# Performance work log

Hardware: AMD Instinct MI355X
Metric: run time of the kernel (lower is better)

Reference implementation:

```python
import jax, jax.numpy as jnp
import numpy as np

EMBED_DIM = 1024
NUM_HEADS = 16
HEAD_DIM = EMBED_DIM // NUM_HEADS
BATCH = 2
SEQ = 2048


def setup_inputs() -> dict:
    key = jax.random.key(0)
    ks = jax.random.split(key, 9)
    scale = 1.0 / np.sqrt(EMBED_DIM)
    return {
        "inputs": jax.random.normal(ks[0], (BATCH, SEQ, EMBED_DIM), jnp.float32),
        "Wq": jax.random.normal(ks[1], (EMBED_DIM, EMBED_DIM), jnp.float32) * scale,
        "bq": jnp.zeros((EMBED_DIM,), jnp.float32),
        "Wk": jax.random.normal(ks[2], (EMBED_DIM, EMBED_DIM), jnp.float32) * scale,
        "bk": jnp.zeros((EMBED_DIM,), jnp.float32),
        "Wv": jax.random.normal(ks[3], (EMBED_DIM, EMBED_DIM), jnp.float32) * scale,
        "bv": jnp.zeros((EMBED_DIM,), jnp.float32),
        "Wo": jax.random.normal(ks[4], (EMBED_DIM, EMBED_DIM), jnp.float32) * scale,
        "bo": jnp.zeros((EMBED_DIM,), jnp.float32),
    }


def reference(inputs, Wq, bq, Wk, bk, Wv, bv, Wo, bo):
    B, S, D = inputs.shape
    H, Dh = NUM_HEADS, HEAD_DIM

    def split_heads(x):  # [B,S,D] -> [B,H,S,Dh]
        return x.reshape(B, S, H, Dh).transpose(0, 2, 1, 3)

    Q = split_heads(inputs @ Wq + bq)
    K = split_heads(inputs @ Wk + bk)
    V = split_heads(inputs @ Wv + bv)

    # naive full-score attention, faithful to the original
    scores = jnp.einsum("bhqd,bhkd->bhqk", Q, K) / jnp.sqrt(jnp.float32(Dh))
    weights = jax.nn.softmax(scores, axis=-1)
    out = jnp.einsum("bhqk,bhkd->bhqd", weights, V)

    concat = out.transpose(0, 2, 1, 3).reshape(B, S, D)
    return concat @ Wo + bo
```

## Files before the change

### kernel.cpp

```cpp
#include <hip/hip_runtime.h>

#define EMBED 1024
#define NHEAD 16
#define HDIM  64
#define BATCH 2
#define SEQ   2048
#define MTOK  (BATCH * SEQ)
#define QSCALE 0.1803368801f

typedef __bf16 bf16x8 __attribute__((ext_vector_type(8)));
typedef float  f32x4  __attribute__((ext_vector_type(4)));

__device__ __forceinline__ unsigned short f2bf(float f) {
  return (unsigned short)((__float_as_uint(f) + 0x8000u) >> 16);
}
__device__ __forceinline__ unsigned int pkbf(float a, float b) {
  unsigned int ua = __float_as_uint(a) + 0x8000u;
  unsigned int ub = __float_as_uint(b) + 0x8000u;
  return __builtin_amdgcn_perm(ub, ua, 0x07060302u);
}

__device__ __forceinline__ void gload_lds16(const unsigned short* g, unsigned short* l) {
  __builtin_amdgcn_global_load_lds((__attribute__((address_space(1))) void*)g,
                                   (__attribute__((address_space(3))) void*)l, 16, 0, 0);
}

__global__ __launch_bounds__(256)
void prep_k(const float* __restrict__ X, unsigned short* __restrict__ Xbf,
            const float* __restrict__ w0, const float* __restrict__ w1,
            const float* __restrict__ w2, const float* __restrict__ w3,
            unsigned short* __restrict__ t0, unsigned short* __restrict__ t1,
            unsigned short* __restrict__ t2, unsigned short* __restrict__ t3) {
  const int id = blockIdx.x;
  if (id < 4096) {
    int i = id * 256 + threadIdx.x;
    float4 f = reinterpret_cast<const float4*>(X)[i];
    reinterpret_cast<uint2*>(Xbf)[i] = make_uint2(pkbf(f.x, f.y), pkbf(f.z, f.w));
    return;
  }
  const int t = id - 4096;
  const float* s; unsigned short* d;
  switch (t >> 8) {
    case 0: s = w0; d = t0; break;
    case 1: s = w1; d = t1; break;
    case 2: s = w2; d = t2; break;
    default: s = w3; d = t3; break;
  }
  const int tt = t & 255;
  const int k0 = (tt >> 4) * 64, n0 = (tt & 15) * 64;
  __shared__ unsigned short T[64][65];
  for (int i = threadIdx.x; i < 4096; i += 256) {
    int r = i >> 6, c = i & 63;
    T[c][r] = f2bf(s[(size_t)(k0 + r) * EMBED + n0 + c]);
  }
  __syncthreads();
  for (int i = threadIdx.x; i < 4096; i += 256) {
    int r = i >> 6, c = i & 63;
    d[(size_t)(n0 + r) * EMBED + k0 + c] = T[r][c];
  }
}

template<int MODE, int BM>
__global__ void gemm_k(const unsigned short* __restrict__ A,
                       const unsigned short* __restrict__ Bt,
                       const float* __restrict__ b0, const float* __restrict__ b1,
                       const float* __restrict__ b2,
                       unsigned short* __restrict__ oQ, unsigned short* __restrict__ oK,
                       unsigned short* __restrict__ oV, float* __restrict__ oF) {
  constexpr int MI = BM / 32;
  constexpr int NT = EMBED / 32;
  constexpr int LPT = BM / 64 + 2;

  __shared__ unsigned short As[3][BM][32];
  __shared__ unsigned short Bs[3][128][32];

  const int tid = threadIdx.x, lane = tid & 63, wave = tid >> 6;
  const int lr = lane & 15, quad = lane >> 4;
  const int wm = (wave >> 1) * (BM / 2), wn = (wave & 1) * 64;
  const int row0 = blockIdx.x * BM, col0 = blockIdx.y * 128;
  const int srow = lane >> 2, sc = lane & 3;
  const int scsw = (sc ^ ((srow >> 1) & 3)) * 8;
  const int sw = (quad ^ ((lr >> 1) & 3)) * 8;

  const f32x4 fz = {0.f, 0.f, 0.f, 0.f};
  f32x4 acc[MI][4];
#pragma unroll
  for (int i = 0; i < MI; ++i)
#pragma unroll
    for (int j = 0; j < 4; ++j) acc[i][j] = fz;

  auto stage = [&](int bufi, int tt) {
#pragma unroll
    for (int g = 0; g < BM / 64; ++g) {
      int rbase = wave * (BM / 4) + g * 16;
      gload_lds16(&A[(size_t)(row0 + rbase + srow) * EMBED + tt * 32 + scsw],
                  &As[bufi][rbase][0]);
    }
#pragma unroll
    for (int g = 0; g < 2; ++g) {
      int rbase = wave * 32 + g * 16;
      gload_lds16(&Bt[(size_t)(col0 + rbase + srow) * EMBED + tt * 32 + scsw],
                  &Bs[bufi][rbase][0]);
    }
  };

  stage(0, 0);
  stage(1, 1);

  int buf = 0, sb = 2;
  for (int t = 0; t < NT; ++t) {
    if (t < NT - 1)
      asm volatile("s_waitcnt vmcnt(%0)" :: "n"(LPT) : "memory");
    else
      asm volatile("s_waitcnt vmcnt(0)" ::: "memory");
    __builtin_amdgcn_s_barrier();

    bf16x8 af[MI], bv[4];
#pragma unroll
    for (int i = 0; i < MI; ++i)
      af[i] = *reinterpret_cast<const bf16x8*>(&As[buf][wm + i * 16 + lr][sw]);
#pragma unroll
    for (int j = 0; j < 4; ++j)
      bv[j] = *reinterpret_cast<const bf16x8*>(&Bs[buf][wn + j * 16 + lr][sw]);

    __builtin_amdgcn_s_setprio(1);
#pragma unroll
    for (int i = 0; i < MI; ++i)
#pragma unroll
      for (int j = 0; j < 4; ++j)
        acc[i][j] = __builtin_amdgcn_mfma_f32_16x16x32_bf16(af[i], bv[j],
                                                            acc[i][j], 0, 0, 0);
    __builtin_amdgcn_s_setprio(0);

    if (t + 2 < NT) stage(sb, t + 2);
    buf = (buf == 2) ? 0 : buf + 1;
    sb  = (sb  == 2) ? 0 : sb  + 1;
  }

#pragma unroll
  for (int i = 0; i < MI; ++i) {
#pragma unroll
    for (int j = 0; j < 4; ++j) {
      const int col = col0 + wn + j * 16 + lr;
      if (MODE == 1) {
        const float bb = b0[col];
#pragma unroll
        for (int r = 0; r < 4; ++r) {
          const int row = row0 + wm + i * 16 + quad * 4 + r;
          oF[((size_t)row << 10) + col] = acc[i][j][r] + bb;
        }
      } else {
        const int which = col >> 10, cn = col & 1023;
        const float bb = (which == 0 ? b0 : which == 1 ? b1 : b2)[cn];
        const float sscale = (which == 0) ? QSCALE : 1.0f;
        const int h = cn >> 6, dd = cn & 63;
#pragma unroll
        for (int r = 0; r < 4; ++r) {
          const int row = row0 + wm + i * 16 + quad * 4 + r;
          const int b = row >> 11, ss = row & (SEQ - 1);
          const float v = (acc[i][j][r] + bb) * sscale;
          if (which == 0) {
            oQ[((((size_t)b * NHEAD + h) * SEQ + ss) << 6) + dd] = f2bf(v);
          } else if (which == 1) {
            oK[((((size_t)b * NHEAD + h) * SEQ + ss) << 6) + dd] = f2bf(v);
          } else {
            oV[(((size_t)b * NHEAD + h) * HDIM + dd) * SEQ + ss] = f2bf(v);
          }
        }
      }
    }
  }
}

__global__ __launch_bounds__(256, 2)
void attn_k(const unsigned short* __restrict__ Qb,
            const unsigned short* __restrict__ Kb,
            const unsigned short* __restrict__ Vt,
            unsigned short* __restrict__ Ctx) {
  __shared__ unsigned short QPs[128][64];
  __shared__ unsigned short Ks[2][64][64];
  __shared__ unsigned short Vs[2][64][64];
  const int tid = threadIdx.x, lane = tid & 63, wave = tid >> 6;
  const int lr = lane & 15, quad = lane >> 4;
  const int bh = blockIdx.x, qt = blockIdx.y;
  const size_t base = (size_t)bh * SEQ * HDIM;
  const int srow = lane >> 3, sc = lane & 7;
  const int sw0 = (quad ^ (lr & 7)) * 8;
  const int sw1 = ((quad ^ 4) ^ (lr & 7)) * 8;

#pragma unroll
  for (int g = 0; g < 4; ++g) {
    int rbase = wave * 32 + g * 8;
    int row = rbase + srow;
    gload_lds16(&Qb[base + (size_t)(qt * 128 + row) * HDIM + ((sc ^ (row & 7)) * 8)],
                &QPs[rbase][0]);
  }
#pragma unroll
  for (int g = 0; g < 2; ++g) {
    int rbase = wave * 16 + g * 8;
    int row = rbase + srow;
    gload_lds16(&Kb[base + (size_t)row * HDIM + ((sc ^ (row & 7)) * 8)],
                &Ks[0][rbase][0]);
    gload_lds16(&Vt[base + (size_t)row * SEQ + ((sc ^ (row & 7)) * 8)],
                &Vs[0][rbase][0]);
  }
  __syncthreads();

  bf16x8 qf[2][2];
#pragma unroll
  for (int g = 0; g < 2; ++g) {
    qf[g][0] = *reinterpret_cast<const bf16x8*>(&QPs[wave * 32 + g * 16 + lr][sw0]);
    qf[g][1] = *reinterpret_cast<const bf16x8*>(&QPs[wave * 32 + g * 16 + lr][sw1]);
  }
  __threadfence_block();

  float l_part[2] = {0.f, 0.f};
  const f32x4 fz = {0.f, 0.f, 0.f, 0.f};
  f32x4 oacc[2][4];
#pragma unroll
  for (int g = 0; g < 2; ++g)
#pragma unroll
    for (int d = 0; d < 4; ++d) oacc[g][d] = fz;

  constexpr int NT = SEQ / 64;
  for (int kt = 0;;) {
    const int buf = kt & 1;

    if (kt + 1 < NT) {
#pragma unroll
      for (int g = 0; g < 2; ++g) {
        int rbase = wave * 16 + g * 8;
        int row = rbase + srow;
        gload_lds16(&Kb[base + (size_t)((kt + 1) * 64 + row) * HDIM + ((sc ^ (row & 7)) * 8)],
                    &Ks[buf ^ 1][rbase][0]);
        gload_lds16(&Vt[base + (size_t)row * SEQ + (kt + 1) * 64 + ((sc ^ (row & 7)) * 8)],
                    &Vs[buf ^ 1][rbase][0]);
      }
    }

    f32x4 sc4[2][4];
#pragma unroll
    for (int nt = 0; nt < 4; ++nt) {
      bf16x8 kf0 = *reinterpret_cast<const bf16x8*>(&Ks[buf][nt * 16 + lr][sw0]);
      bf16x8 kf1 = *reinterpret_cast<const bf16x8*>(&Ks[buf][nt * 16 + lr][sw1]);
#pragma unroll
      for (int g = 0; g < 2; ++g) {
        f32x4 a = __builtin_amdgcn_mfma_f32_16x16x32_bf16(kf0, qf[g][0], fz, 0, 0, 0);
        sc4[g][nt] = __builtin_amdgcn_mfma_f32_16x16x32_bf16(kf1, qf[g][1], a, 0, 0, 0);
      }
    }

#pragma unroll
    for (int g = 0; g < 2; ++g)
#pragma unroll
      for (int nt = 0; nt < 4; ++nt) {
        float p0 = __builtin_amdgcn_exp2f(sc4[g][nt][0]);
        float p1 = __builtin_amdgcn_exp2f(sc4[g][nt][1]);
        float p2 = __builtin_amdgcn_exp2f(sc4[g][nt][2]);
        float p3 = __builtin_amdgcn_exp2f(sc4[g][nt][3]);
        l_part[g] += (p0 + p1) + (p2 + p3);
        const int pc = (nt * 2 + (quad >> 1)) ^ (lr & 7);
        *reinterpret_cast<uint2*>(&QPs[wave * 32 + g * 16 + lr][pc * 8 + (quad & 1) * 4]) =
            make_uint2(pkbf(p0, p1), pkbf(p2, p3));
      }

    __threadfence_block();

    bf16x8 pa[2][2];
#pragma unroll
    for (int g = 0; g < 2; ++g) {
      pa[g][0] = *reinterpret_cast<const bf16x8*>(&QPs[wave * 32 + g * 16 + lr][sw0]);
      pa[g][1] = *reinterpret_cast<const bf16x8*>(&QPs[wave * 32 + g * 16 + lr][sw1]);
    }
#pragma unroll
    for (int d = 0; d < 4; ++d) {
      bf16x8 vb0 = *reinterpret_cast<const bf16x8*>(&Vs[buf][d * 16 + lr][sw0]);
      bf16x8 vb1 = *reinterpret_cast<const bf16x8*>(&Vs[buf][d * 16 + lr][sw1]);
#pragma unroll
      for (int g = 0; g < 2; ++g) {
        oacc[g][d] = __builtin_amdgcn_mfma_f32_16x16x32_bf16(pa[g][0], vb0, oacc[g][d], 0, 0, 0);
        oacc[g][d] = __builtin_amdgcn_mfma_f32_16x16x32_bf16(pa[g][1], vb1, oacc[g][d], 0, 0, 0);
      }
    }

    if (++kt == NT) break;
    __syncthreads();
  }

#pragma unroll
  for (int g = 0; g < 2; ++g) {
    l_part[g] += __shfl_xor(l_part[g], 16);
    l_part[g] += __shfl_xor(l_part[g], 32);
  }

  const int b = bh >> 4, h = bh & 15;
#pragma unroll
  for (int g = 0; g < 2; ++g) {
    float linv[4];
#pragma unroll
    for (int r = 0; r < 4; ++r) linv[r] = 1.0f / __shfl(l_part[g], quad * 4 + r);
#pragma unroll
    for (int d = 0; d < 4; ++d)
#pragma unroll
      for (int r = 0; r < 4; ++r) {
        const int q = qt * 128 + wave * 32 + g * 16 + quad * 4 + r;
        Ctx[(((size_t)b * SEQ + q) << 10) + h * 64 + d * 16 + lr] =
            f2bf(oacc[g][d][r] * linv[r]);
      }
  }
}

extern "C" void kernel_launch(void* const* d_in, const int* in_sizes, int n_in,
                              void* d_out, int out_size, void* d_ws, size_t ws_size,
                              hipStream_t stream) {
  const float* X  = (const float*)d_in[0];
  const float* Wq = (const float*)d_in[1];
  const float* bq = (const float*)d_in[2];
  const float* Wk = (const float*)d_in[3];
  const float* bk = (const float*)d_in[4];
  const float* Wv = (const float*)d_in[5];
  const float* bv = (const float*)d_in[6];
  const float* Wo = (const float*)d_in[7];
  const float* bo = (const float*)d_in[8];

  unsigned short* ws = (unsigned short*)d_ws;
  const size_t M1 = (size_t)1024 * 1024;
  unsigned short* Xbf = ws;
  unsigned short* WqT = ws + 4 * M1;
  unsigned short* WkT = ws + 5 * M1;
  unsigned short* WvT = ws + 6 * M1;
  unsigned short* WoT = ws + 7 * M1;
  unsigned short* Qb  = ws + 8 * M1;
  unsigned short* Kb  = ws + 12 * M1;
  unsigned short* Vt  = ws + 16 * M1;
  unsigned short* Ctx = ws + 20 * M1;

  prep_k<<<5120, 256, 0, stream>>>(X, Xbf, Wq, Wk, Wv, Wo, WqT, WkT, WvT, WoT);

  gemm_k<0, 128><<<dim3(MTOK / 128, 3072 / 128), 256, 0, stream>>>(
      Xbf, WqT, bq, bk, bv, Qb, Kb, Vt, nullptr);

  attn_k<<<dim3(BATCH * NHEAD, SEQ / 128), 256, 0, stream>>>(Qb, Kb, Vt, Ctx);

  gemm_k<1, 64><<<dim3(MTOK / 64, EMBED / 128), 256, 0, stream>>>(
      Ctx, WoT, bo, nullptr, nullptr, nullptr, nullptr, nullptr, (float*)d_out);
}
```

Baseline: 189.1 us.

## Keep softmax probabilities in registers and feed 16x16x16 MFMA directly

Instead of writing exponentiated scores to LDS and reading them back as bf16x8 operands, the probabilities are packed into registers in the layout the QK^T MFMA output already has. They are consumed by 16x16x16 bf16 MFMAs, with the V fragments loaded to match. This removes the LDS round trip and the block fences for P. The cost is twice as many, smaller MFMA instructions and narrower V reads from LDS.

```diff
diff --git a/kernel.cpp b/kernel.cpp
--- a/kernel.cpp
+++ b/kernel.cpp
@@ -10,6 +10,7 @@
 
 typedef __bf16 bf16x8 __attribute__((ext_vector_type(8)));
 typedef float  f32x4  __attribute__((ext_vector_type(4)));
+typedef short  s16x4  __attribute__((ext_vector_type(4)));
 
 __device__ __forceinline__ unsigned short f2bf(float f) {
   return (unsigned short)((__float_as_uint(f) + 0x8000u) >> 16);
@@ -18,6 +19,16 @@
   unsigned int ua = __float_as_uint(a) + 0x8000u;
   unsigned int ub = __float_as_uint(b) + 0x8000u;
   return __builtin_amdgcn_perm(ub, ua, 0x07060302u);
+}
+
+__device__ __forceinline__ f32x4 mfma16(s16x4 a, s16x4 b, f32x4 c) {
+#if __has_builtin(__builtin_amdgcn_mfma_f32_16x16x16bf16_1k)
+  return __builtin_amdgcn_mfma_f32_16x16x16bf16_1k(a, b, c, 0, 0, 0);
+#else
+  f32x4 d = c;
+  asm("v_mfma_f32_16x16x16_bf16 %0, %1, %2, %0" : "+v"(d) : "v"(a), "v"(b));
+  return d;
+#endif
 }
 
 __device__ __forceinline__ void gload_lds16(const unsigned short* g, unsigned short* l) {
@@ -187,6 +198,7 @@
   const int srow = lane >> 3, sc = lane & 7;
   const int sw0 = (quad ^ (lr & 7)) * 8;
   const int sw1 = ((quad ^ 4) ^ (lr & 7)) * 8;
+  const int vq2 = quad >> 1, vh4 = (quad & 1) * 4, vx = lr & 7;
 
 #pragma unroll
   for (int g = 0; g < 4; ++g) {
@@ -212,7 +224,6 @@
     qf[g][0] = *reinterpret_cast<const bf16x8*>(&QPs[wave * 32 + g * 16 + lr][sw0]);
     qf[g][1] = *reinterpret_cast<const bf16x8*>(&QPs[wave * 32 + g * 16 + lr][sw1]);
   }
-  __threadfence_block();
 
   float l_part[2] = {0.f, 0.f};
   const f32x4 fz = {0.f, 0.f, 0.f, 0.f};
@@ -250,36 +261,31 @@
       }
     }
 
+    s16x4 pf[2][4];
 #pragma unroll
     for (int g = 0; g < 2; ++g)
 #pragma unroll
-      for (int nt = 0; nt < 4; ++nt) {
-        float p0 = __builtin_amdgcn_exp2f(sc4[g][nt][0]);
-        float p1 = __builtin_amdgcn_exp2f(sc4[g][nt][1]);
-        float p2 = __builtin_amdgcn_exp2f(sc4[g][nt][2]);
-        float p3 = __builtin_amdgcn_exp2f(sc4[g][nt][3]);
+      for (int kb = 0; kb < 4; ++kb) {
+        float p0 = __builtin_amdgcn_exp2f(sc4[g][kb][0]);
+        float p1 = __builtin_amdgcn_exp2f(sc4[g][kb][1]);
+        float p2 = __builtin_amdgcn_exp2f(sc4[g][kb][2]);
+        float p3 = __builtin_amdgcn_exp2f(sc4[g][kb][3]);
         l_part[g] += (p0 + p1) + (p2 + p3);
-        const int pc = (nt * 2 + (quad >> 1)) ^ (lr & 7);
-        *reinterpret_cast<uint2*>(&QPs[wave * 32 + g * 16 + lr][pc * 8 + (quad & 1) * 4]) =
-            make_uint2(pkbf(p0, p1), pkbf(p2, p3));
-      }
-
-    __threadfence_block();
-
-    bf16x8 pa[2][2];
-#pragma unroll
-    for (int g = 0; g < 2; ++g) {
-      pa[g][0] = *reinterpret_cast<const bf16x8*>(&QPs[wave * 32 + g * 16 + lr][sw0]);
-      pa[g][1] = *reinterpret_cast<const bf16x8*>(&QPs[wave * 32 + g * 16 + lr][sw1]);
-    }
+        uint2 w = make_uint2(pkbf(p0, p1), pkbf(p2, p3));
+        pf[g][kb] = *reinterpret_cast<s16x4*>(&w);
+      }
+
 #pragma unroll
     for (int d = 0; d < 4; ++d) {
-      bf16x8 vb0 = *reinterpret_cast<const bf16x8*>(&Vs[buf][d * 16 + lr][sw0]);
-      bf16x8 vb1 = *reinterpret_cast<const bf16x8*>(&Vs[buf][d * 16 + lr][sw1]);
-#pragma unroll
-      for (int g = 0; g < 2; ++g) {
-        oacc[g][d] = __builtin_amdgcn_mfma_f32_16x16x32_bf16(pa[g][0], vb0, oacc[g][d], 0, 0, 0);
-        oacc[g][d] = __builtin_amdgcn_mfma_f32_16x16x32_bf16(pa[g][1], vb1, oacc[g][d], 0, 0, 0);
+      const unsigned short* vrow = &Vs[buf][d * 16 + lr][0];
+#pragma unroll
+      for (int kb = 0; kb < 4; ++kb) {
+        uint2 vv = *reinterpret_cast<const uint2*>(
+            &vrow[(((kb * 2 + vq2) ^ vx) * 8) + vh4]);
+        s16x4 vb = *reinterpret_cast<s16x4*>(&vv);
+#pragma unroll
+        for (int g = 0; g < 2; ++g)
+          oacc[g][d] = mfma16(pf[g][kb], vb, oacc[g][d]);
       }
     }
 
```

New measurement: 190.9 us. No clear change (+0.9%).

## Load Q, K and V fragments directly from global memory instead of LDS staging

Applied to the files above, without the earlier changes.

The attention kernel stops staging Q, K and V tiles in shared memory through double-buffered async global-to-LDS loads, and each wave now reads its MFMA fragments directly from global memory. Only the P tile stays in LDS. This removes the per-iteration block barrier and the LDS traffic and cuts shared-memory footprint, which could allow more resident blocks. In exchange, every wave fetches the same K/V rows separately through the caches, and there is no explicit prefetch, so memory latency is exposed inside the loop.

```diff
diff --git a/kernel.cpp b/kernel.cpp
--- a/kernel.cpp
+++ b/kernel.cpp
@@ -177,42 +177,22 @@
             const unsigned short* __restrict__ Kb,
             const unsigned short* __restrict__ Vt,
             unsigned short* __restrict__ Ctx) {
-  __shared__ unsigned short QPs[128][64];
-  __shared__ unsigned short Ks[2][64][64];
-  __shared__ unsigned short Vs[2][64][64];
+  __shared__ unsigned short Ps[128][64];
   const int tid = threadIdx.x, lane = tid & 63, wave = tid >> 6;
   const int lr = lane & 15, quad = lane >> 4;
   const int bh = blockIdx.x, qt = blockIdx.y;
   const size_t base = (size_t)bh * SEQ * HDIM;
-  const int srow = lane >> 3, sc = lane & 7;
   const int sw0 = (quad ^ (lr & 7)) * 8;
   const int sw1 = ((quad ^ 4) ^ (lr & 7)) * 8;
 
-#pragma unroll
-  for (int g = 0; g < 4; ++g) {
-    int rbase = wave * 32 + g * 8;
-    int row = rbase + srow;
-    gload_lds16(&Qb[base + (size_t)(qt * 128 + row) * HDIM + ((sc ^ (row & 7)) * 8)],
-                &QPs[rbase][0]);
-  }
+  bf16x8 qf[2][2];
 #pragma unroll
   for (int g = 0; g < 2; ++g) {
-    int rbase = wave * 16 + g * 8;
-    int row = rbase + srow;
-    gload_lds16(&Kb[base + (size_t)row * HDIM + ((sc ^ (row & 7)) * 8)],
-                &Ks[0][rbase][0]);
-    gload_lds16(&Vt[base + (size_t)row * SEQ + ((sc ^ (row & 7)) * 8)],
-                &Vs[0][rbase][0]);
-  }
-  __syncthreads();
-
-  bf16x8 qf[2][2];
-#pragma unroll
-  for (int g = 0; g < 2; ++g) {
-    qf[g][0] = *reinterpret_cast<const bf16x8*>(&QPs[wave * 32 + g * 16 + lr][sw0]);
-    qf[g][1] = *reinterpret_cast<const bf16x8*>(&QPs[wave * 32 + g * 16 + lr][sw1]);
-  }
-  __threadfence_block();
+    const unsigned short* qrow =
+        &Qb[base + (size_t)(qt * 128 + wave * 32 + g * 16 + lr) * HDIM];
+    qf[g][0] = *reinterpret_cast<const bf16x8*>(&qrow[quad * 8]);
+    qf[g][1] = *reinterpret_cast<const bf16x8*>(&qrow[(quad ^ 4) * 8]);
+  }
 
   float l_part[2] = {0.f, 0.f};
   const f32x4 fz = {0.f, 0.f, 0.f, 0.f};
@@ -223,26 +203,14 @@
     for (int d = 0; d < 4; ++d) oacc[g][d] = fz;
 
   constexpr int NT = SEQ / 64;
-  for (int kt = 0;;) {
-    const int buf = kt & 1;
-
-    if (kt + 1 < NT) {
-#pragma unroll
-      for (int g = 0; g < 2; ++g) {
-        int rbase = wave * 16 + g * 8;
-        int row = rbase + srow;
-        gload_lds16(&Kb[base + (size_t)((kt + 1) * 64 + row) * HDIM + ((sc ^ (row & 7)) * 8)],
-                    &Ks[buf ^ 1][rbase][0]);
-        gload_lds16(&Vt[base + (size_t)row * SEQ + (kt + 1) * 64 + ((sc ^ (row & 7)) * 8)],
-                    &Vs[buf ^ 1][rbase][0]);
-      }
-    }
-
+  for (int kt = 0; kt < NT; ++kt) {
     f32x4 sc4[2][4];
 #pragma unroll
     for (int nt = 0; nt < 4; ++nt) {
-      bf16x8 kf0 = *reinterpret_cast<const bf16x8*>(&Ks[buf][nt * 16 + lr][sw0]);
-      bf16x8 kf1 = *reinterpret_cast<const bf16x8*>(&Ks[buf][nt * 16 + lr][sw1]);
+      const unsigned short* krow =
+          &Kb[base + (size_t)(kt * 64 + nt * 16 + lr) * HDIM];
+      bf16x8 kf0 = *reinterpret_cast<const bf16x8*>(&krow[quad * 8]);
+      bf16x8 kf1 = *reinterpret_cast<const bf16x8*>(&krow[(quad ^ 4) * 8]);
 #pragma unroll
       for (int g = 0; g < 2; ++g) {
         f32x4 a = __builtin_amdgcn_mfma_f32_16x16x32_bf16(kf0, qf[g][0], fz, 0, 0, 0);
@@ -260,7 +228,7 @@
         float p3 = __builtin_amdgcn_exp2f(sc4[g][nt][3]);
         l_part[g] += (p0 + p1) + (p2 + p3);
         const int pc = (nt * 2 + (quad >> 1)) ^ (lr & 7);
-        *reinterpret_cast<uint2*>(&QPs[wave * 32 + g * 16 + lr][pc * 8 + (quad & 1) * 4]) =
+        *reinterpret_cast<uint2*>(&Ps[wave * 32 + g * 16 + lr][pc * 8 + (quad & 1) * 4]) =
             make_uint2(pkbf(p0, p1), pkbf(p2, p3));
       }
 
@@ -269,22 +237,21 @@
     bf16x8 pa[2][2];
 #pragma unroll
     for (int g = 0; g < 2; ++g) {
-      pa[g][0] = *reinterpret_cast<const bf16x8*>(&QPs[wave * 32 + g * 16 + lr][sw0]);
-      pa[g][1] = *reinterpret_cast<const bf16x8*>(&QPs[wave * 32 + g * 16 + lr][sw1]);
+      pa[g][0] = *reinterpret_cast<const bf16x8*>(&Ps[wave * 32 + g * 16 + lr][sw0]);
+      pa[g][1] = *reinterpret_cast<const bf16x8*>(&Ps[wave * 32 + g * 16 + lr][sw1]);
     }
 #pragma unroll
     for (int d = 0; d < 4; ++d) {
-      bf16x8 vb0 = *reinterpret_cast<const bf16x8*>(&Vs[buf][d * 16 + lr][sw0]);
-      bf16x8 vb1 = *reinterpret_cast<const bf16x8*>(&Vs[buf][d * 16 + lr][sw1]);
+      const unsigned short* vrow =
+          &Vt[base + (size_t)(d * 16 + lr) * SEQ + kt * 64];
+      bf16x8 vb0 = *reinterpret_cast<const bf16x8*>(&vrow[quad * 8]);
+      bf16x8 vb1 = *reinterpret_cast<const bf16x8*>(&vrow[(quad ^ 4) * 8]);
 #pragma unroll
       for (int g = 0; g < 2; ++g) {
         oacc[g][d] = __builtin_amdgcn_mfma_f32_16x16x32_bf16(pa[g][0], vb0, oacc[g][d], 0, 0, 0);
         oacc[g][d] = __builtin_amdgcn_mfma_f32_16x16x32_bf16(pa[g][1], vb1, oacc[g][d], 0, 0, 0);
       }
     }
-
-    if (++kt == NT) break;
-    __syncthreads();
   }
 
 #pragma unroll
```

Measured after the change: 258.8 us. 36.9% more time.

## Add dedicated 128x192-tile QKV projection GEMM with split-phase staging

Applied to the files above, without the earlier changes.

Replaces the QKV projection GEMM with a specialized kernel using 128x192 output tiles, so each wave computes a 64x96 sub-tile. That improves A-operand reuse and cuts the grid from 768 to 512 blocks. Each K-step is split into two MFMA halves, with the next stage's global-to-LDS loads interleaved between them and extra barriers. The output GEMM keeps the old kernel with the QKV mode removed. Risks include higher register and LDS use, lower occupancy, more barriers per iteration, and worse wave balance across CUs.

```diff
diff --git a/kernel.cpp b/kernel.cpp
--- a/kernel.cpp
+++ b/kernel.cpp
@@ -60,13 +60,144 @@
   }
 }
 
-template<int MODE, int BM>
+__global__ __launch_bounds__(256)
+void gemmq_k(const unsigned short* __restrict__ A,
+             const unsigned short* __restrict__ Bt,
+             const float* __restrict__ b0, const float* __restrict__ b1,
+             const float* __restrict__ b2,
+             unsigned short* __restrict__ oQ, unsigned short* __restrict__ oK,
+             unsigned short* __restrict__ oV) {
+  constexpr int NT = EMBED / 32;
+
+  __shared__ unsigned short As[3][128][32];
+  __shared__ unsigned short Bs[3][192][32];
+
+  const int tid = threadIdx.x, lane = tid & 63, wave = tid >> 6;
+  const int lr = lane & 15, quad = lane >> 4;
+  const int wm = (wave >> 1) * 64, wn = (wave & 1) * 96;
+  const int row0 = blockIdx.x * 128, col0 = blockIdx.y * 192;
+  const int srow = lane >> 2, sc = lane & 3;
+  const int scsw = (sc ^ ((srow >> 1) & 3)) * 8;
+  const int sw = (quad ^ ((lr >> 1) & 3)) * 8;
+
+  const f32x4 fz = {0.f, 0.f, 0.f, 0.f};
+  f32x4 acc[4][6];
+#pragma unroll
+  for (int i = 0; i < 4; ++i)
+#pragma unroll
+    for (int j = 0; j < 6; ++j) acc[i][j] = fz;
+
+  auto stage = [&](int bufi, int tt) {
+#pragma unroll
+    for (int g = 0; g < 2; ++g) {
+      int rbase = wave * 32 + g * 16;
+      gload_lds16(&A[(size_t)(row0 + rbase + srow) * EMBED + tt * 32 + scsw],
+                  &As[bufi][rbase][0]);
+    }
+#pragma unroll
+    for (int g = 0; g < 3; ++g) {
+      int rbase = wave * 48 + g * 16;
+      gload_lds16(&Bt[(size_t)(col0 + rbase + srow) * EMBED + tt * 32 + scsw],
+                  &Bs[bufi][rbase][0]);
+    }
+  };
+
+  stage(0, 0);
+  stage(1, 1);
+
+  int rb = 0, sb = 2;
+  for (int t = 0; t < NT; ++t) {
+    if (t < NT - 1)
+      asm volatile("s_waitcnt vmcnt(5)" ::: "memory");
+    else
+      asm volatile("s_waitcnt vmcnt(0)" ::: "memory");
+    __builtin_amdgcn_s_barrier();
+
+    bf16x8 af[4], bv[3];
+#pragma unroll
+    for (int i = 0; i < 4; ++i)
+      af[i] = *reinterpret_cast<const bf16x8*>(&As[rb][wm + i * 16 + lr][sw]);
+#pragma unroll
+    for (int j = 0; j < 3; ++j)
+      bv[j] = *reinterpret_cast<const bf16x8*>(&Bs[rb][wn + j * 16 + lr][sw]);
+    if (t + 2 < NT) {
+#pragma unroll
+      for (int g = 0; g < 2; ++g) {
+        int rbase = wave * 32 + g * 16;
+        gload_lds16(&A[(size_t)(row0 + rbase + srow) * EMBED + (t + 2) * 32 + scsw],
+                    &As[sb][rbase][0]);
+      }
+      gload_lds16(&Bt[(size_t)(col0 + wave * 48 + srow) * EMBED + (t + 2) * 32 + scsw],
+                  &Bs[sb][wave * 48][0]);
+    }
+    __builtin_amdgcn_s_setprio(1);
+#pragma unroll
+    for (int i = 0; i < 4; ++i)
+#pragma unroll
+      for (int j = 0; j < 3; ++j)
+        acc[i][j] = __builtin_amdgcn_mfma_f32_16x16x32_bf16(af[i], bv[j],
+                                                            acc[i][j], 0, 0, 0);
+    __builtin_amdgcn_s_setprio(0);
+    __builtin_amdgcn_s_barrier();
+
+    bf16x8 bw[3];
+#pragma unroll
+    for (int j = 0; j < 3; ++j)
+      bw[j] = *reinterpret_cast<const bf16x8*>(&Bs[rb][wn + (j + 3) * 16 + lr][sw]);
+    if (t + 2 < NT) {
+#pragma unroll
+      for (int g = 1; g < 3; ++g) {
+        int rbase = wave * 48 + g * 16;
+        gload_lds16(&Bt[(size_t)(col0 + rbase + srow) * EMBED + (t + 2) * 32 + scsw],
+                    &Bs[sb][rbase][0]);
+      }
+    }
+    __builtin_amdgcn_s_barrier();
+    __builtin_amdgcn_s_setprio(1);
+#pragma unroll
+    for (int i = 0; i < 4; ++i)
+#pragma unroll
+      for (int j = 0; j < 3; ++j)
+        acc[i][j + 3] = __builtin_amdgcn_mfma_f32_16x16x32_bf16(af[i], bw[j],
+                                                                acc[i][j + 3], 0, 0, 0);
+    __builtin_amdgcn_s_setprio(0);
+    __builtin_amdgcn_s_barrier();
+
+    rb = (rb == 2) ? 0 : rb + 1;
+    sb = (sb == 2) ? 0 : sb + 1;
+  }
+
+#pragma unroll
+  for (int i = 0; i < 4; ++i) {
+#pragma unroll
+    for (int j = 0; j < 6; ++j) {
+      const int col = col0 + wn + j * 16 + lr;
+      const int which = col >> 10, cn = col & 1023;
+      const float bb = (which == 0 ? b0 : which == 1 ? b1 : b2)[cn];
+      const float sscale = (which == 0) ? QSCALE : 1.0f;
+      const int h = cn >> 6, dd = cn & 63;
+#pragma unroll
+      for (int r = 0; r < 4; ++r) {
+        const int row = row0 + wm + i * 16 + quad * 4 + r;
+        const int b = row >> 11, ss = row & (SEQ - 1);
+        const float v = (acc[i][j][r] + bb) * sscale;
+        if (which == 0) {
+          oQ[((((size_t)b * NHEAD + h) * SEQ + ss) << 6) + dd] = f2bf(v);
+        } else if (which == 1) {
+          oK[((((size_t)b * NHEAD + h) * SEQ + ss) << 6) + dd] = f2bf(v);
+        } else {
+          oV[(((size_t)b * NHEAD + h) * HDIM + dd) * SEQ + ss] = f2bf(v);
+        }
+      }
+    }
+  }
+}
+
+template<int BM>
 __global__ void gemm_k(const unsigned short* __restrict__ A,
                        const unsigned short* __restrict__ Bt,
-                       const float* __restrict__ b0, const float* __restrict__ b1,
-                       const float* __restrict__ b2,
-                       unsigned short* __restrict__ oQ, unsigned short* __restrict__ oK,
-                       unsigned short* __restrict__ oV, float* __restrict__ oF) {
+                       const float* __restrict__ b0,
+                       float* __restrict__ oF) {
   constexpr int MI = BM / 32;
   constexpr int NT = EMBED / 32;
   constexpr int LPT = BM / 64 + 2;
@@ -142,31 +273,11 @@
 #pragma unroll
     for (int j = 0; j < 4; ++j) {
       const int col = col0 + wn + j * 16 + lr;
-      if (MODE == 1) {
-        const float bb = b0[col];
-#pragma unroll
-        for (int r = 0; r < 4; ++r) {
-          const int row = row0 + wm + i * 16 + quad * 4 + r;
-          oF[((size_t)row << 10) + col] = acc[i][j][r] + bb;
-        }
-      } else {
-        const int which = col >> 10, cn = col & 1023;
-        const float bb = (which == 0 ? b0 : which == 1 ? b1 : b2)[cn];
-        const float sscale = (which == 0) ? QSCALE : 1.0f;
-        const int h = cn >> 6, dd = cn & 63;
-#pragma unroll
-        for (int r = 0; r < 4; ++r) {
-          const int row = row0 + wm + i * 16 + quad * 4 + r;
-          const int b = row >> 11, ss = row & (SEQ - 1);
-          const float v = (acc[i][j][r] + bb) * sscale;
-          if (which == 0) {
-            oQ[((((size_t)b * NHEAD + h) * SEQ + ss) << 6) + dd] = f2bf(v);
-          } else if (which == 1) {
-            oK[((((size_t)b * NHEAD + h) * SEQ + ss) << 6) + dd] = f2bf(v);
-          } else {
-            oV[(((size_t)b * NHEAD + h) * HDIM + dd) * SEQ + ss] = f2bf(v);
-          }
-        }
+      const float bb = b0[col];
+#pragma unroll
+      for (int r = 0; r < 4; ++r) {
+        const int row = row0 + wm + i * 16 + quad * 4 + r;
+        oF[((size_t)row << 10) + col] = acc[i][j][r] + bb;
       }
     }
   }
@@ -337,11 +448,11 @@
 
   prep_k<<<5120, 256, 0, stream>>>(X, Xbf, Wq, Wk, Wv, Wo, WqT, WkT, WvT, WoT);
 
-  gemm_k<0, 128><<<dim3(MTOK / 128, 3072 / 128), 256, 0, stream>>>(
-      Xbf, WqT, bq, bk, bv, Qb, Kb, Vt, nullptr);
+  gemmq_k<<<dim3(MTOK / 128, 3072 / 192), 256, 0, stream>>>(
+      Xbf, WqT, bq, bk, bv, Qb, Kb, Vt);
 
   attn_k<<<dim3(BATCH * NHEAD, SEQ / 128), 256, 0, stream>>>(Qb, Kb, Vt, Ctx);
 
-  gemm_k<1, 64><<<dim3(MTOK / 64, EMBED / 128), 256, 0, stream>>>(
-      Ctx, WoT, bo, nullptr, nullptr, nullptr, nullptr, nullptr, (float*)d_out);
-}
+  gemm_k<64><<<dim3(MTOK / 64, EMBED / 128), 256, 0, stream>>>(
+      Ctx, WoT, bo, (float*)d_out);
+}
```

Result: no change. 191.7 us (+1.3%).
